# Kernel tuning notes

Measured on AMD Instinct MI355X. Metric: run time of the kernel, lower is better.

## Reference

```python
import jax, jax.numpy as jnp
import numpy as np

W = 1024          # hpm.W (Fourier window size)
D = 2 * W         # real-ified dimension
BATCH = 2048
P = 8             # number of previous windows
OMEGA = 50        # sparsity level kept by hard threshold
N_ITERS = 10
L = 1.0           # hpm.L (Lipschitz constant, non-learnable)
CLAMP = 150.0


def setup_inputs() -> dict:
    key = jax.random.key(0)
    k1, k2, k3 = jax.random.split(key, 3)
    x = jax.random.normal(k1, (BATCH, D), jnp.float32)
    prev_windows = jax.random.normal(k2, (P, BATCH, D), jnp.float32)
    # learnable dictionary (Fourier-initialized in the original; random orthogonal-ish here)
    W_d = jax.random.normal(k3, (D, D), jnp.float32) / np.float32(np.sqrt(D))
    # S = I - (1/L) W_d^T W_d, exactly as in __init__
    S = jnp.eye(D, dtype=jnp.float32) - (1.0 / L) * (W_d.T @ W_d)
    lambda2 = jnp.array(1.0, jnp.float32)
    return {"x": x, "prev_windows": prev_windows, "W_d": W_d, "S": S, "lambda2": lambda2}


def _hard_thr(v):
    # keep the OMEGA largest-|.| entries along the last axis, zero the rest
    a = jnp.abs(v)
    kth = jax.lax.top_k(a, OMEGA)[0][..., -1:]  # (batch, 1) threshold
    return jnp.where(a >= kth, v, jnp.zeros_like(v))


def reference(x, prev_windows, W_d, S, lambda2):
    # B = (1/L) W_d x         (batch, D); z vectors kept as (batch, D), last dim == the
    # original dim=-2 since trailing singleton dim is squeezed away.
    B = (1.0 / L) * jnp.einsum('ij,bj->bi', W_d, x)
    z = _hard_thr(B)
    z = _hard_thr(B + jnp.einsum('ij,bj->bi', S, z))

    # attention over previous windows
    s_t = jnp.einsum('ji,bj->bi', W_d, z)                       # W_d^T z : (batch, D)
    s_prev = jnp.einsum('ij,pbj->pbi', W_d, prev_windows)       # (P, batch, D)
    # diagonal of (P,batch,batch) matmul == per-(p,b) dot product; compute it directly
    att = jnp.einsum('pbd,bd->pb', s_prev, s_t)                 # (P, batch)
    att = jax.nn.softmax(att, axis=1)
    pw = jnp.clip(prev_windows, -CLAMP, CLAMP)
    z = lambda2 * jnp.sum(pw * att[..., None], axis=0)          # (batch, D)

    # LIHT iterations; only zs[-1] is used downstream, so carry only the last z
    def step(zc, _):
        zn = _hard_thr(B + jnp.einsum('ij,bj->bi', S, zc))
        return zn, None
    z_last, _ = jax.lax.scan(step, z, None, length=N_ITERS)

    # complex power spectrum: sign flip on imag part does not change the norm
    cpx = z_last.reshape(BATCH, 2, W)
    p = cpx[:, 0, :] ** 2 + cpx[:, 1, :] ** 2                   # (batch, W)
    mD = p.sum(0)                                               # (W,)
    mD_norm = (mD - mD.min()) / (mD.max() - mD.min() + 1e-8)
    return mD_norm, z_last
```

## Files before the change

kernel.cpp:

```cpp
#include <hip/hip_runtime.h>


#define DD 2048
#define NB 2048
#define PLANE ((size_t)1 << 22)

using short8v  = __attribute__((ext_vector_type(8))) short;
using ushort8v = __attribute__((ext_vector_type(8))) unsigned short;
using ushort4v = __attribute__((ext_vector_type(4))) unsigned short;
using float4v  = __attribute__((ext_vector_type(4))) float;

__device__ __forceinline__ unsigned short f2bf(float f) {
  unsigned u = __float_as_uint(f);
  u = u + 0x7fffu + ((u >> 16) & 1u);
  return (unsigned short)(u >> 16);
}
__device__ __forceinline__ float bf2f(unsigned short h) {
  return __uint_as_float((unsigned)h << 16);
}
__device__ __forceinline__ void gload16(const void* g, void* l) {
  __builtin_amdgcn_global_load_lds((const __attribute__((address_space(1))) void*)g,
                                   (__attribute__((address_space(3))) void*)l,
                                   16, 0, 0);
}

template<int R>
__global__ __launch_bounds__(256)
void conv3T(const float* __restrict__ in, unsigned short* __restrict__ p0,
            unsigned short* __restrict__ p1, unsigned short* __restrict__ p2) {
  __shared__ unsigned short lds3[3][4][R][8];
  const int rt = blockIdx.x, c = blockIdx.y, t = threadIdx.x;
  const int cf = (t & 7) * 4;
  const int g = cf >> 3, e0 = cf & 7;
#pragma unroll
  for (int pass = 0; pass < R / 32; ++pass) {
    const int r = pass * 32 + (t >> 3);
    float4 v = *(const float4*)(in + (size_t)(rt * R + r) * DD + c * 32 + cf);
    float vv[4] = {v.x, v.y, v.z, v.w};
    ushort4v o0, o1, o2;
#pragma unroll
    for (int j = 0; j < 4; ++j) {
      unsigned short a0 = f2bf(vv[j]); float r1 = vv[j] - bf2f(a0);
      unsigned short a1 = f2bf(r1);    float r2 = r1 - bf2f(a1);
      unsigned short a2 = f2bf(r2);
      o0[j] = a0; o1[j] = a1; o2[j] = a2;
    }
    *(ushort4v*)&lds3[0][g][r][e0] = o0;
    *(ushort4v*)&lds3[1][g][r][e0] = o1;
    *(ushort4v*)&lds3[2][g][r][e0] = o2;
  }
  __syncthreads();
  const ushort8v* src = (const ushort8v*)lds3;
  const size_t tb = ((size_t)rt * 64 + c) * (R * 32);
#pragma unroll
  for (int w = 0; w < (3 * R) / 64; ++w) {
    const int idx = w * 256 + t;
    const int p = idx / (4 * R), off = idx % (4 * R);
    unsigned short* dst = (p == 0 ? p0 : p == 1 ? p1 : p2) + tb + (size_t)off * 8;
    *(ushort8v*)dst = src[idx];
  }
}

__global__ __launch_bounds__(256)
void tconv3(const float* __restrict__ in, unsigned short* __restrict__ p0,
            unsigned short* __restrict__ p1, unsigned short* __restrict__ p2) {
  __shared__ unsigned short lds3[3][4][64][8];
  const int nt = blockIdx.x, c = blockIdx.y, t = threadIdx.x;
  const int nf = (t & 15) * 4;
#pragma unroll
  for (int pass = 0; pass < 2; ++pass) {
    const int kr = pass * 16 + (t >> 4);
    float4 v = *(const float4*)(in + (size_t)(c * 32 + kr) * DD + nt * 64 + nf);
    float vv[4] = {v.x, v.y, v.z, v.w};
    const int g = kr >> 3, e = kr & 7;
#pragma unroll
    for (int j = 0; j < 4; ++j) {
      unsigned short a0 = f2bf(vv[j]); float r1 = vv[j] - bf2f(a0);
      unsigned short a1 = f2bf(r1);    float r2 = r1 - bf2f(a1);
      unsigned short a2 = f2bf(r2);
      lds3[0][g][nf + j][e] = a0;
      lds3[1][g][nf + j][e] = a1;
      lds3[2][g][nf + j][e] = a2;
    }
  }
  __syncthreads();
  const ushort8v* src = (const ushort8v*)lds3;
  const size_t tb = ((size_t)nt * 64 + c) * 2048;
#pragma unroll
  for (int w = 0; w < 3; ++w) {
    const int idx = w * 256 + t;
    const int p = idx >> 8, off = idx & 255;
    unsigned short* dst = (p == 0 ? p0 : p == 1 ? p1 : p2) + tb + (size_t)off * 8;
    *(ushort8v*)dst = src[idx];
  }
}

#define LDS_B_OFF 24576
#define LDS_BUF   36864

template<int ADD>
__global__ __launch_bounds__(256, 2)
void gemm_bf6(const unsigned short* __restrict__ PA,
              const unsigned short* __restrict__ PB,
              const float* __restrict__ Cadd, float* __restrict__ Cout) {
  __shared__ char lds[2 * LDS_BUF];
  const int tid = threadIdx.x, lane = tid & 63, wid = tid >> 6;

  int lin = (int)blockIdx.x;
  lin = (lin & 7) * 64 + (lin >> 3);
  const int m0 = (lin >> 5) * 128;
  const int n0 = (lin & 31) * 64;

  auto stage = [&](char* base, int c) {
    const size_t at = ((size_t)(m0 >> 7) * 64 + c) * 4096;
    const size_t bt = ((size_t)(n0 >> 6) * 64 + c) * 2048;
#pragma unroll
    for (int i = 0; i < 6; ++i) {
      const int tA = wid * 6 + i, p = tA >> 3, j = tA & 7;
      gload16(PA + p * PLANE + at + j * 512 + lane * 8,
              base + p * 8192 + j * 1024 + lane * 16);
    }
#pragma unroll
    for (int i = 0; i < 3; ++i) {
      const int tB = wid * 3 + i, p = tB >> 2, j = tB & 3;
      gload16(PB + p * PLANE + bt + j * 512 + lane * 8,
              base + LDS_B_OFF + p * 4096 + j * 1024 + lane * 16);
    }
  };

  float4v acc[4][2] = {};

  const int rsel = (wid >> 1) * 64;
  const int csel = (wid & 1) * 32;
  const int g16  = lane >> 4;
  const int l15  = lane & 15;
  const int aoff = g16 * 2048 + (rsel + l15) * 16;
  const int boff = LDS_B_OFF + g16 * 1024 + (csel + l15) * 16;

  stage(lds, 0);
  __syncthreads();

  for (int c = 0; c < 64; ++c) {
    char* cur = lds + (c & 1) * LDS_BUF;
    if (c < 63) stage(lds + ((c & 1) ^ 1) * LDS_BUF, c + 1);

    short8v b0[2], b1[2], b2[2];
#pragma unroll
    for (int ng = 0; ng < 2; ++ng) {
      b0[ng] = *(const short8v*)(cur + boff + 0 * 4096 + ng * 256);
      b1[ng] = *(const short8v*)(cur + boff + 1 * 4096 + ng * 256);
      b2[ng] = *(const short8v*)(cur + boff + 2 * 4096 + ng * 256);
    }
#pragma unroll
    for (int mg = 0; mg < 4; ++mg) {
      const short8v a0 = *(const short8v*)(cur + 0 * 8192 + aoff + mg * 256);
      const short8v a1 = *(const short8v*)(cur + 1 * 8192 + aoff + mg * 256);
      const short8v a2 = *(const short8v*)(cur + 2 * 8192 + aoff + mg * 256);
#pragma unroll
      for (int ng = 0; ng < 2; ++ng) {
        float4v t = acc[mg][ng];
        t = __builtin_amdgcn_mfma_f32_16x16x32_bf16(a0, b0[ng], t, 0, 0, 0);
        t = __builtin_amdgcn_mfma_f32_16x16x32_bf16(a0, b1[ng], t, 0, 0, 0);
        t = __builtin_amdgcn_mfma_f32_16x16x32_bf16(a1, b0[ng], t, 0, 0, 0);
        t = __builtin_amdgcn_mfma_f32_16x16x32_bf16(a1, b1[ng], t, 0, 0, 0);
        t = __builtin_amdgcn_mfma_f32_16x16x32_bf16(a0, b2[ng], t, 0, 0, 0);
        t = __builtin_amdgcn_mfma_f32_16x16x32_bf16(a2, b0[ng], t, 0, 0, 0);
        acc[mg][ng] = t;
      }
    }
    __syncthreads();
  }

  const int row0 = m0 + rsel + g16 * 4;
  const int col0 = n0 + csel + l15;
#pragma unroll
  for (int mg = 0; mg < 4; ++mg)
#pragma unroll
    for (int ng = 0; ng < 2; ++ng)
#pragma unroll
      for (int r = 0; r < 4; ++r) {
        const size_t o = (size_t)(row0 + mg * 16 + r) * DD + col0 + ng * 16;
        float v = acc[mg][ng][r];
        if (ADD) v += Cadd[o];
        Cout[o] = v;
      }
}

template<int HASBASE>
__global__ __launch_bounds__(64)
void spapply_sl(const float* __restrict__ M, const float* __restrict__ baseB,
                float* __restrict__ outF, const unsigned* __restrict__ sidx,
                const float* __restrict__ sval, const int* __restrict__ scnt) {
  const int b = blockIdx.y, lane = threadIdx.x;
  const int col = blockIdx.x * 256 + lane * 4;
  const int nc = scnt[b];
  const unsigned* ip = sidx + b * 64;
  const float* vp = sval + b * 64;
  const size_t ro = (size_t)b * DD + col;
  float4 a;
  if (HASBASE) a = *(const float4*)&baseB[ro];
  else         a = make_float4(0.f, 0.f, 0.f, 0.f);
  for (int t = 0; t < nc; ++t) {
    const unsigned j = ip[t];
    const float v = vp[t];
    float4 m = *(const float4*)&M[(size_t)j * DD + col];
    a.x = fmaf(v, m.x, a.x); a.y = fmaf(v, m.y, a.y);
    a.z = fmaf(v, m.z, a.z); a.w = fmaf(v, m.w, a.w);
  }
  *(float4*)&outF[ro] = a;
}

__global__ __launch_bounds__(64)
void topk_kernel(const float* __restrict__ src, unsigned* __restrict__ sidx,
                 float* __restrict__ sval, int* __restrict__ scnt,
                 float* __restrict__ dense, float* __restrict__ mD,
                 int finalMode) {
  const int b = blockIdx.x;
  const int lane = threadIdx.x;
  const float* row = src + (size_t)b * DD;
  float v[32]; unsigned ab[32];
#pragma unroll
  for (int e4 = 0; e4 < 8; ++e4) {
    float4 t = *(const float4*)&row[e4*256 + lane*4];
    v[e4*4+0]=t.x; v[e4*4+1]=t.y; v[e4*4+2]=t.z; v[e4*4+3]=t.w;
  }
#pragma unroll
  for (int e = 0; e < 32; ++e) ab[e] = __float_as_uint(v[e]) & 0x7fffffffu;

  unsigned mxb = 0;
#pragma unroll
  for (int e = 0; e < 32; ++e) mxb = ab[e] > mxb ? ab[e] : mxb;
  for (int off = 32; off; off >>= 1) {
    unsigned o = (unsigned)__shfl_down((int)mxb, off);
    mxb = o > mxb ? o : mxb;
  }
  mxb = (unsigned)__shfl((int)mxb, 0);
  const int emax = (int)(mxb >> 23);

  int eStar = 0, cntAbove = 0;
  {
    int prevc = 0;
    for (int e = emax; e >= 0; --e) {
      unsigned T = ((unsigned)e) << 23;
      int c = 0;
#pragma unroll
      for (int k = 0; k < 32; ++k) c += (ab[k] >= T) ? 1 : 0;
      for (int off = 32; off; off >>= 1) c += __shfl_down(c, off);
      c = __shfl(c, 0);
      if (c >= 50) { eStar = e; cntAbove = prevc; break; }
      prevc = c;
    }
  }
  unsigned kth = ((unsigned)eStar) << 23;
  int kneed = 50 - cntAbove;

  __shared__ int hist[256];
  __shared__ int sh_sel, sh_kneed;
  for (int p = 0; p < 3; ++p) {
    const unsigned mask = (p==0) ? 0x7F800000u : (p==1) ? 0x7FFF8000u : 0x7FFFFF80u;
    const int sh = (p==0) ? 15 : (p==1) ? 7 : 0;
    for (int t = lane; t < 256; t += 64) hist[t] = 0;
    __syncthreads();
#pragma unroll
    for (int e = 0; e < 32; ++e)
      if ((ab[e] & mask) == kth) atomicAdd(&hist[(ab[e] >> sh) & 0xFF], 1);
    __syncthreads();
    int h0 = hist[lane*4+0], h1 = hist[lane*4+1], h2 = hist[lane*4+2], h3 = hist[lane*4+3];
    int s = h0 + h1 + h2 + h3;
    int x = s;
    for (int off = 1; off < 64; off <<= 1) {
      int y = __shfl_down(x, off);
      if (lane + off < 64) x += y;
    }
    int excl = x - s;
    int c3 = excl + h3, c2 = c3 + h2, c1 = c2 + h1, c0 = c1 + h0;
    if (c0 >= kneed && c1   < kneed) { sh_sel = lane*4+0; sh_kneed = kneed - c1;  }
    if (c1 >= kneed && c2   < kneed) { sh_sel = lane*4+1; sh_kneed = kneed - c2;  }
    if (c2 >= kneed && c3   < kneed) { sh_sel = lane*4+2; sh_kneed = kneed - c3;  }
    if (c3 >= kneed && excl < kneed) { sh_sel = lane*4+3; sh_kneed = kneed - excl;}
    __syncthreads();
    kth |= ((unsigned)sh_sel) << sh;
    kneed = sh_kneed;
    __syncthreads();
  }

  int base = 0;
#pragma unroll
  for (int e4 = 0; e4 < 8; ++e4) {
    float o[4];
#pragma unroll
    for (int qq = 0; qq < 4; ++qq) {
      const int e = e4*4 + qq;
      const bool sel = ab[e] >= kth;
      unsigned long long msk = __ballot(sel);
      int pre = __popcll(msk & ((1ull << lane) - 1ull));
      const unsigned gi = (unsigned)(e4*256 + lane*4 + qq);
      if (sel) {
        int slot = base + pre;
        if (slot < 64) { sidx[b*64+slot] = gi; sval[b*64+slot] = v[e]; }
        if (finalMode) atomicAdd(&mD[gi & 1023u], v[e]*v[e]);
      }
      base += __popcll(msk);
      o[qq] = sel ? v[e] : 0.f;
    }
    if (finalMode) {
      float4 t = {o[0],o[1],o[2],o[3]};
      *(float4*)&dense[(size_t)b*DD + e4*256 + lane*4] = t;
    }
  }
  if (lane == 0) scnt[b] = base < 64 ? base : 64;
}

__global__ __launch_bounds__(256)
void attdot_kernel(const float* __restrict__ prev, const float* __restrict__ U,
                   float* __restrict__ att) {
  const int b = blockIdx.x, p = blockIdx.y, tid = threadIdx.x;
  const float* pr = prev + ((size_t)p*NB + b) * DD;
  const float* u  = U + (size_t)b * DD;
  float s = 0.f;
#pragma unroll
  for (int h = 0; h < 2; ++h) {
    int i = (tid + h*256) * 4;
    float4 a = *(const float4*)&pr[i];
    float4 c = *(const float4*)&u[i];
    s += a.x*c.x + a.y*c.y + a.z*c.z + a.w*c.w;
  }
  for (int off = 32; off; off >>= 1) s += __shfl_down(s, off);
  __shared__ float ps[4];
  if ((tid & 63) == 0) ps[tid >> 6] = s;
  __syncthreads();
  if (tid == 0) att[(size_t)p*NB + b] = ps[0]+ps[1]+ps[2]+ps[3];
}

__global__ __launch_bounds__(256)
void softmax_kernel(const float* __restrict__ att, float* __restrict__ attw) {
  const int p = blockIdx.x, tid = threadIdx.x;
  const float* a = att + (size_t)p*NB;
  float loc[8]; float mx = -3.4e38f;
#pragma unroll
  for (int h = 0; h < 8; ++h) { loc[h] = a[tid + h*256]; mx = fmaxf(mx, loc[h]); }
  for (int off = 32; off; off >>= 1) mx = fmaxf(mx, __shfl_down(mx, off));
  __shared__ float ps[4]; __shared__ float sh_m, sh_s;
  if ((tid & 63) == 0) ps[tid >> 6] = mx;
  __syncthreads();
  if (tid == 0) sh_m = fmaxf(fmaxf(ps[0],ps[1]), fmaxf(ps[2],ps[3]));
  __syncthreads();
  const float m = sh_m;
  float sum = 0.f;
#pragma unroll
  for (int h = 0; h < 8; ++h) sum += expf(loc[h] - m);
  for (int off = 32; off; off >>= 1) sum += __shfl_down(sum, off);
  __syncthreads();
  if ((tid & 63) == 0) ps[tid >> 6] = sum;
  __syncthreads();
  if (tid == 0) sh_s = ps[0]+ps[1]+ps[2]+ps[3];
  __syncthreads();
  const float inv = 1.0f / sh_s;
#pragma unroll
  for (int h = 0; h < 8; ++h) attw[(size_t)p*NB + tid + h*256] = expf(loc[h] - m) * inv;
}

__global__ __launch_bounds__(256)
void zatt_kernel(const float* __restrict__ prev, const float* __restrict__ attw,
                 const float* __restrict__ lam, float* __restrict__ Z) {
  const int b = blockIdx.x, tid = threadIdx.x;
  __shared__ float w[8];
  if (tid < 8) w[tid] = attw[(size_t)tid*NB + b];
  __syncthreads();
  const float l2 = lam[0];
#pragma unroll
  for (int h = 0; h < 2; ++h) {
    int i = (tid + h*256) * 4;
    float4 acc = {0.f,0.f,0.f,0.f};
#pragma unroll
    for (int p = 0; p < 8; ++p) {
      float4 pv = *(const float4*)&prev[((size_t)p*NB + b)*DD + i];
      float wp = w[p];
      acc.x += wp * fminf(fmaxf(pv.x, -150.f), 150.f);
      acc.y += wp * fminf(fmaxf(pv.y, -150.f), 150.f);
      acc.z += wp * fminf(fmaxf(pv.z, -150.f), 150.f);
      acc.w += wp * fminf(fmaxf(pv.w, -150.f), 150.f);
    }
    acc.x *= l2; acc.y *= l2; acc.z *= l2; acc.w *= l2;
    *(float4*)&Z[(size_t)b*DD + i] = acc;
  }
}

__global__ __launch_bounds__(256)
void norm_kernel(float* __restrict__ mD) {
  const int tid = threadIdx.x;
  float v[4]; float mn = 3.4e38f, mx = -3.4e38f;
#pragma unroll
  for (int h = 0; h < 4; ++h) {
    v[h] = mD[tid + h*256];
    mn = fminf(mn, v[h]); mx = fmaxf(mx, v[h]);
  }
  for (int off = 32; off; off >>= 1) {
    mn = fminf(mn, __shfl_down(mn, off));
    mx = fmaxf(mx, __shfl_down(mx, off));
  }
  __shared__ float pmn[4], pmx[4]; __shared__ float smn, smx;
  if ((tid & 63) == 0) { pmn[tid>>6] = mn; pmx[tid>>6] = mx; }
  __syncthreads();
  if (tid == 0) {
    smn = fminf(fminf(pmn[0],pmn[1]), fminf(pmn[2],pmn[3]));
    smx = fmaxf(fmaxf(pmx[0],pmx[1]), fmaxf(pmx[2],pmx[3]));
  }
  __syncthreads();
  const float d = smx - smn + 1e-8f;
#pragma unroll
  for (int h = 0; h < 4; ++h) mD[tid + h*256] = (v[h] - smn) / d;
}

extern "C" void kernel_launch(void* const* d_in, const int* in_sizes, int n_in,
                              void* d_out, int out_size, void* d_ws, size_t ws_size,
                              hipStream_t stream) {
  const float* x    = (const float*)d_in[0];
  const float* prev = (const float*)d_in[1];
  const float* Wd   = (const float*)d_in[2];
  const float* S    = (const float*)d_in[3];
  const float* lam  = (const float*)d_in[4];

  float* out   = (float*)d_out;
  float* mD    = out;
  float* zlast = out + 1024;

  float* B  = (float*)d_ws;
  float* C  = B  + (1u << 22);
  float* X1 = C  + (1u << 22);
  unsigned* sidx = (unsigned*)(X1 + (1u << 22));
  float*    sval = (float*)(sidx + 2048*64);
  int*      scnt = (int*)(sval + 2048*64);
  float*    att  = (float*)(scnt + 2048);
  float*    attw = att + 8*2048;
  unsigned short* PA = (unsigned short*)(attw + 8*2048);
  unsigned short* PB = PA + 3 * PLANE;
  float* U = zlast;

  const dim3 gSp(8, NB);
  const dim3 gA(16, 64);
  const dim3 gB(32, 64);

  conv3T<128><<<gA, 256, 0, stream>>>(x,  PA, PA + PLANE, PA + 2*PLANE);
  conv3T<64> <<<gB, 256, 0, stream>>>(Wd, PB, PB + PLANE, PB + 2*PLANE);
  gemm_bf6<0><<<512, 256, 0, stream>>>(PA, PB, nullptr, B);
  topk_kernel<<<NB, 64, 0, stream>>>(B, sidx, sval, scnt, nullptr, nullptr, 0);
  spapply_sl<1><<<gSp, 64, 0, stream>>>(S, B, C, sidx, sval, scnt);
  topk_kernel<<<NB, 64, 0, stream>>>(C, sidx, sval, scnt, nullptr, nullptr, 0);
  spapply_sl<0><<<gSp, 64, 0, stream>>>(Wd, nullptr, X1, sidx, sval, scnt);
  conv3T<128><<<gA, 256, 0, stream>>>(X1, PA, PA + PLANE, PA + 2*PLANE);
  tconv3<<<gB, 256, 0, stream>>>(Wd, PB, PB + PLANE, PB + 2*PLANE);
  gemm_bf6<0><<<512, 256, 0, stream>>>(PA, PB, nullptr, U);
  attdot_kernel<<<dim3(NB, 8), 256, 0, stream>>>(prev, U, att);
  softmax_kernel<<<8, 256, 0, stream>>>(att, attw);
  zatt_kernel<<<NB, 256, 0, stream>>>(prev, attw, lam, X1);
  conv3T<128><<<gA, 256, 0, stream>>>(X1, PA, PA + PLANE, PA + 2*PLANE);
  conv3T<64> <<<gB, 256, 0, stream>>>(S,  PB, PB + PLANE, PB + 2*PLANE);
  gemm_bf6<1><<<512, 256, 0, stream>>>(PA, PB, B, C);
  topk_kernel<<<NB, 64, 0, stream>>>(C, sidx, sval, scnt, nullptr, nullptr, 0);
  for (int it = 1; it < 10; ++it) {
    spapply_sl<1><<<gSp, 64, 0, stream>>>(S, B, C, sidx, sval, scnt);
    const int fin = (it == 9);
    if (fin) hipMemsetAsync(mD, 0, 1024 * sizeof(float), stream);
    topk_kernel<<<NB, 64, 0, stream>>>(C, sidx, sval, scnt,
                                       fin ? zlast : nullptr,
                                       fin ? mD : nullptr, fin);
  }
  norm_kernel<<<1, 256, 0, stream>>>(mD);
}
```

Measured before the change: 1.221 ms.

## Enlarge GEMM tile to 128x128 with 512 threads and triple-buffered LDS pipeline

The three bf16x3 GEMMs now use 128x128 output tiles computed by 8 waves per block (256 blocks), instead of 128x64 tiles with 4 waves (512 blocks). Staging moves from double to triple buffering: loads run two chunks ahead, with explicit vmcnt waits and raw s_barrier in place of __syncthreads. Loading is split so four waves fetch A and four fetch B. The block-to-tile mapping is also regrouped per XCD for L2 locality. This aims to cut global and LDS traffic per FLOP and to hide load latency, at the cost of more LDS per block (144KB) and possibly fewer resident blocks per CU.

```diff
diff --git a/kernel.cpp b/kernel.cpp
--- a/kernel.cpp
+++ b/kernel.cpp
@@ -4,6 +4,7 @@
 #define DD 2048
 #define NB 2048
 #define PLANE ((size_t)1 << 22)
+#define ZONE 49152
 
 using short8v  = __attribute__((ext_vector_type(8))) short;
 using ushort8v = __attribute__((ext_vector_type(8))) unsigned short;
@@ -95,61 +96,70 @@
   }
 }
 
-#define LDS_B_OFF 24576
-#define LDS_BUF   36864
-
 template<int ADD>
-__global__ __launch_bounds__(256, 2)
+__global__ __launch_bounds__(512)
 void gemm_bf6(const unsigned short* __restrict__ PA,
               const unsigned short* __restrict__ PB,
               const float* __restrict__ Cadd, float* __restrict__ Cout) {
-  __shared__ char lds[2 * LDS_BUF];
+  __shared__ char lds[3 * ZONE];
   const int tid = threadIdx.x, lane = tid & 63, wid = tid >> 6;
 
-  int lin = (int)blockIdx.x;
-  lin = (lin & 7) * 64 + (lin >> 3);
-  const int m0 = (lin >> 5) * 128;
-  const int n0 = (lin & 31) * 64;
+  const int lin = (int)blockIdx.x;
+  const int xcd = lin & 7, q = lin >> 3;
+  const int mt = (xcd >> 1) * 4 + (q >> 3);
+  const int nt = (xcd & 1) * 8 + (q & 7);
+  const int m0 = mt * 128, n0 = nt * 128;
 
   auto stage = [&](char* base, int c) {
-    const size_t at = ((size_t)(m0 >> 7) * 64 + c) * 4096;
-    const size_t bt = ((size_t)(n0 >> 6) * 64 + c) * 2048;
-#pragma unroll
-    for (int i = 0; i < 6; ++i) {
-      const int tA = wid * 6 + i, p = tA >> 3, j = tA & 7;
-      gload16(PA + p * PLANE + at + j * 512 + lane * 8,
-              base + p * 8192 + j * 1024 + lane * 16);
-    }
-#pragma unroll
-    for (int i = 0; i < 3; ++i) {
-      const int tB = wid * 3 + i, p = tB >> 2, j = tB & 3;
-      gload16(PB + p * PLANE + bt + j * 512 + lane * 8,
-              base + LDS_B_OFF + p * 4096 + j * 1024 + lane * 16);
+    if (wid < 4) {
+      const size_t at = ((size_t)mt * 64 + c) * 4096;
+#pragma unroll
+      for (int i = 0; i < 6; ++i) {
+        const int slot = wid * 6 + i, p = slot >> 3, j = slot & 7;
+        gload16(PA + p * PLANE + at + j * 512 + lane * 8,
+                base + p * 8192 + j * 1024 + lane * 16);
+      }
+    } else {
+#pragma unroll
+      for (int i = 0; i < 6; ++i) {
+        const int b = (wid - 4) * 6 + i, p = b >> 3, r = b & 7;
+        const int sub = r >> 2, j = r & 3;
+        const size_t bt = ((size_t)(nt * 2 + sub) * 64 + c) * 2048;
+        gload16(PB + p * PLANE + bt + j * 512 + lane * 8,
+                base + 24576 + p * 8192 + sub * 4096 + j * 1024 + lane * 16);
+      }
     }
   };
 
   float4v acc[4][2] = {};
 
-  const int rsel = (wid >> 1) * 64;
-  const int csel = (wid & 1) * 32;
+  const int rsel = (wid >> 2) * 64;
+  const int csel = (wid & 3) * 32;
   const int g16  = lane >> 4;
   const int l15  = lane & 15;
   const int aoff = g16 * 2048 + (rsel + l15) * 16;
-  const int boff = LDS_B_OFF + g16 * 1024 + (csel + l15) * 16;
+  const int boff = 24576 + (csel >> 6) * 4096 + g16 * 1024
+                 + ((csel & 32) + l15) * 16;
 
   stage(lds, 0);
-  __syncthreads();
-
+  stage(lds + ZONE, 1);
+
+  int zc = 0, zs = 2;
   for (int c = 0; c < 64; ++c) {
-    char* cur = lds + (c & 1) * LDS_BUF;
-    if (c < 63) stage(lds + ((c & 1) ^ 1) * LDS_BUF, c + 1);
-
+    if (c + 2 < 64) stage(lds + zs * ZONE, c + 2);
+    if (c + 2 < 64)      asm volatile("s_waitcnt vmcnt(12)" ::: "memory");
+    else if (c + 1 < 64) asm volatile("s_waitcnt vmcnt(6)"  ::: "memory");
+    else                 asm volatile("s_waitcnt vmcnt(0)"  ::: "memory");
+    __builtin_amdgcn_s_barrier();
+    __builtin_amdgcn_sched_barrier(0);
+
+    const char* cur = lds + zc * ZONE;
     short8v b0[2], b1[2], b2[2];
 #pragma unroll
     for (int ng = 0; ng < 2; ++ng) {
-      b0[ng] = *(const short8v*)(cur + boff + 0 * 4096 + ng * 256);
-      b1[ng] = *(const short8v*)(cur + boff + 1 * 4096 + ng * 256);
-      b2[ng] = *(const short8v*)(cur + boff + 2 * 4096 + ng * 256);
+      b0[ng] = *(const short8v*)(cur + boff + 0 * 8192 + ng * 256);
+      b1[ng] = *(const short8v*)(cur + boff + 1 * 8192 + ng * 256);
+      b2[ng] = *(const short8v*)(cur + boff + 2 * 8192 + ng * 256);
     }
 #pragma unroll
     for (int mg = 0; mg < 4; ++mg) {
@@ -168,7 +178,10 @@
         acc[mg][ng] = t;
       }
     }
-    __syncthreads();
+    __builtin_amdgcn_sched_barrier(0);
+    __builtin_amdgcn_s_barrier();
+    zc = (zc == 2) ? 0 : zc + 1;
+    zs = (zs == 2) ? 0 : zs + 1;
   }
 
   const int row0 = m0 + rsel + g16 * 4;
@@ -443,20 +456,20 @@
 
   conv3T<128><<<gA, 256, 0, stream>>>(x,  PA, PA + PLANE, PA + 2*PLANE);
   conv3T<64> <<<gB, 256, 0, stream>>>(Wd, PB, PB + PLANE, PB + 2*PLANE);
-  gemm_bf6<0><<<512, 256, 0, stream>>>(PA, PB, nullptr, B);
+  gemm_bf6<0><<<256, 512, 0, stream>>>(PA, PB, nullptr, B);
   topk_kernel<<<NB, 64, 0, stream>>>(B, sidx, sval, scnt, nullptr, nullptr, 0);
   spapply_sl<1><<<gSp, 64, 0, stream>>>(S, B, C, sidx, sval, scnt);
   topk_kernel<<<NB, 64, 0, stream>>>(C, sidx, sval, scnt, nullptr, nullptr, 0);
   spapply_sl<0><<<gSp, 64, 0, stream>>>(Wd, nullptr, X1, sidx, sval, scnt);
   conv3T<128><<<gA, 256, 0, stream>>>(X1, PA, PA + PLANE, PA + 2*PLANE);
   tconv3<<<gB, 256, 0, stream>>>(Wd, PB, PB + PLANE, PB + 2*PLANE);
-  gemm_bf6<0><<<512, 256, 0, stream>>>(PA, PB, nullptr, U);
+  gemm_bf6<0><<<256, 512, 0, stream>>>(PA, PB, nullptr, U);
   attdot_kernel<<<dim3(NB, 8), 256, 0, stream>>>(prev, U, att);
   softmax_kernel<<<8, 256, 0, stream>>>(att, attw);
   zatt_kernel<<<NB, 256, 0, stream>>>(prev, attw, lam, X1);
   conv3T<128><<<gA, 256, 0, stream>>>(X1, PA, PA + PLANE, PA + 2*PLANE);
   conv3T<64> <<<gB, 256, 0, stream>>>(S,  PB, PB + PLANE, PB + 2*PLANE);
-  gemm_bf6<1><<<512, 256, 0, stream>>>(PA, PB, B, C);
+  gemm_bf6<1><<<256, 512, 0, stream>>>(PA, PB, B, C);
   topk_kernel<<<NB, 64, 0, stream>>>(C, sidx, sval, scnt, nullptr, nullptr, 0);
   for (int it = 1; it < 10; ++it) {
     spapply_sl<1><<<gSp, 64, 0, stream>>>(S, B, C, sidx, sval, scnt);
```

After: 1.218 ms. No clear change (-0.2%).
